# Performance work log

Measured on AMD Instinct MI355X. Metric: run time of the kernel, lower is better.

Reference implementation:

```python
import jax, jax.numpy as jnp
import numpy as np

DIM = 25
N_NODES = 20000
N_EDGES = 320000
NFEAT = 300
NHID = 64
NCLASS = 50


def setup_inputs() -> dict:
    key = jax.random.key(0)
    ks = jax.random.split(key, 8)
    s1 = np.sqrt(6.0 / (NFEAT + NHID))
    s2 = np.sqrt(6.0 / (NHID * DIM + NCLASS))
    return {
        "x": jax.random.normal(ks[0], (N_NODES, NFEAT), dtype=jnp.float32),
        "adj_rows": jax.random.randint(ks[1], (DIM, N_EDGES), 0, N_NODES, dtype=jnp.int32),
        "adj_cols": jax.random.randint(ks[2], (DIM, N_EDGES), 0, N_NODES, dtype=jnp.int32),
        "adj_vals": jax.random.uniform(ks[3], (DIM, N_EDGES), dtype=jnp.float32),
        "W1": jax.random.uniform(ks[4], (DIM, NFEAT, NHID), dtype=jnp.float32, minval=-s1, maxval=s1),
        "b1": jnp.zeros((DIM, NHID), dtype=jnp.float32),
        "W2": jax.random.uniform(ks[5], (DIM, NHID * DIM, NCLASS), dtype=jnp.float32, minval=-s2, maxval=s2),
        "b2": jnp.zeros((DIM, NCLASS), dtype=jnp.float32),
    }


def _spmm(rows, cols, vals, sup, n):
    # sparse [n,n] @ dense [n,f] via gather + segment-sum scatter-add
    return jax.ops.segment_sum(vals[:, None] * sup[cols], rows, num_segments=n)


def reference(x, adj_rows, adj_cols, adj_vals, W1, b1, W2, b2):
    n = x.shape[0]
    spmm = jax.vmap(lambda r, c, v, s: _spmm(r, c, v, s, n))
    # layer 1: per-branch dense mm, spmm, bias, relu  -> [DIM, n, NHID]
    sup1 = jnp.einsum("nf,dfh->dnh", x, W1)
    h1 = jax.nn.relu(spmm(adj_rows, adj_cols, adj_vals, sup1) + b1[:, None, :])
    # permute + reshape: concat branch features per node -> [n, DIM*NHID]
    h1cat = jnp.transpose(h1, (1, 0, 2)).reshape(n, -1)
    # layer 2: per-branch dense mm, spmm, bias, relu -> [DIM, n, NCLASS]
    sup2 = jnp.einsum("nk,dkc->dnc", h1cat, W2)
    h2 = jax.nn.relu(spmm(adj_rows, adj_cols, adj_vals, sup2) + b2[:, None, :])
    # max-pool over branches (POOLING='max')
    return jnp.max(h2, axis=0)
```

## Files before the change

### kernel.cpp

```cpp
#include <hip/hip_runtime.h>
#include <hip/hip_bf16.h>
#include <cstdint>
#include <cstddef>

#define DIM 25
#define NN 20000
#define NE 320000
#define NF 300
#define NH 64
#define NC 50
#define K2 (DIM*NH)
#define KP1 320
#define B1T_ROWS 1664
#define B2T_ROWS 1280
#define NBK 79
#define EPB 4096
#define BPB ((NE + EPB - 1) / EPB)
#define FCAP 5632

typedef __attribute__((ext_vector_type(8))) short short8;
typedef __attribute__((ext_vector_type(4))) float floatx4;
typedef __hip_bfloat16 bf16;

static __device__ __forceinline__ unsigned bf16bits(float f) {
    bf16 b = __float2bfloat16(f);
    return (unsigned)*reinterpret_cast<unsigned short*>(&b);
}
static __device__ __forceinline__ float blo(unsigned w) { return __uint_as_float(w << 16); }
static __device__ __forceinline__ float bhi(unsigned w) { return __uint_as_float(w & 0xFFFF0000u); }

static __device__ __forceinline__ void gld16(const void* g, void* l) {
    __builtin_amdgcn_global_load_lds((const __attribute__((address_space(1))) unsigned*)g,
                                     (__attribute__((address_space(3))) unsigned*)l, 16, 0, 0);
}

__global__ void zero_kernel(int* __restrict__ p, int n) {
    int i = blockIdx.x * blockDim.x + threadIdx.x;
    if (i < n) p[i] = 0;
}

__global__ __launch_bounds__(256) void bucket_scatter_kernel(const int* __restrict__ rows,
                                                             const int* __restrict__ cols,
                                                             const float* __restrict__ vals,
                                                             int* __restrict__ gcur,
                                                             unsigned* __restrict__ interE,
                                                             unsigned char* __restrict__ interR) {
    const int d = blockIdx.y;
    const int e0 = blockIdx.x * EPB;
    __shared__ int lh[NBK];
    __shared__ int lo[NBK];
    __shared__ int lbase[NBK];
    __shared__ unsigned entE[EPB];
    __shared__ unsigned short entR[EPB];
    const int tid = threadIdx.x;
    for (int i = tid; i < NBK; i += 256) lh[i] = 0;
    __syncthreads();
    const int* rd = rows + (size_t)d * NE;
    const int* cd = cols + (size_t)d * NE;
    const float* vd = vals + (size_t)d * NE;
    const int e1 = min(e0 + EPB, NE);
    const int ne = e1 - e0;
    for (int i = e0 + tid; i < e1; i += 256)
        atomicAdd(&lh[rd[i] >> 8], 1);
    __syncthreads();
    if (tid == 0) {
        int run = 0;
        for (int b = 0; b < NBK; ++b) { lo[b] = run; run += lh[b]; }
    }
    __syncthreads();
    for (int i = tid; i < NBK; i += 256) {
        lbase[i] = lh[i] ? atomicAdd(&gcur[d * NBK + i], lh[i]) : 0;
        lh[i] = 0;
    }
    __syncthreads();
    for (int i = e0 + tid; i < e1; i += 256) {
        int r = rd[i];
        int b = r >> 8;
        int rank = atomicAdd(&lh[b], 1);
        int pos = lo[b] + rank;
        entE[pos] = (unsigned)cd[i] | (bf16bits(vd[i]) << 16);
        entR[pos] = (unsigned short)r;
    }
    __syncthreads();
    for (int p = tid; p < ne; p += 256) {
        int r = entR[p];
        int b = r >> 8;
        int gpos = lbase[b] + (p - lo[b]);
        if (gpos < FCAP) {
            size_t slot = ((size_t)d * NBK + b) * FCAP + gpos;
            interE[slot] = entE[p];
            interR[slot] = (unsigned char)r;
        }
    }
}

__global__ void bucket_scan_kernel(const int* __restrict__ gcur,
                                   int* __restrict__ offs_b,
                                   int* __restrict__ bcnt,
                                   int* __restrict__ offs) {
    const int d = blockIdx.x;
    if (threadIdx.x != 0) return;
    int run = 0;
    for (int b = 0; b < NBK; ++b) {
        int c = min(gcur[d * NBK + b], FCAP);
        offs_b[d * NBK + b] = run;
        bcnt[d * NBK + b] = c;
        run += c;
    }
    offs[d * (NN + 1) + NN] = run;
}

__global__ __launch_bounds__(256) void csr_finalize_kernel(const unsigned* __restrict__ interE,
                                                           const unsigned char* __restrict__ interR,
                                                           const int* __restrict__ offs_b,
                                                           const int* __restrict__ bcnt,
                                                           int* __restrict__ offs,
                                                           unsigned* __restrict__ sedge) {
    const int d = blockIdx.y;
    const int b = blockIdx.x;
    const int tid = threadIdx.x;
    const int s = offs_b[d * NBK + b];
    const int cnt = bcnt[d * NBK + b];
    const size_t base = ((size_t)d * NBK + b) * FCAP;
    __shared__ int sm[256];
    __shared__ int cur[256];
    __shared__ unsigned lse[FCAP];
    sm[tid] = 0;
    __syncthreads();
    for (int i = tid; i < cnt; i += 256)
        atomicAdd(&sm[interR[base + i]], 1);
    __syncthreads();
    int own = sm[tid];
    for (int off = 1; off < 256; off <<= 1) {
        int t = (tid >= off) ? sm[tid - off] : 0;
        __syncthreads();
        sm[tid] += t;
        __syncthreads();
    }
    int excl = sm[tid] - own;
    int row = (b << 8) + tid;
    if (row < NN) offs[d * (NN + 1) + row] = s + excl;
    cur[tid] = excl;
    __syncthreads();
    for (int i = tid; i < cnt; i += 256) {
        int idx = atomicAdd(&cur[interR[base + i]], 1);
        lse[idx] = interE[base + i];
    }
    __syncthreads();
    unsigned* sed = sedge + (size_t)d * NE;
    for (int t = tid; t < cnt; t += 256)
        sed[s + t] = lse[t];
}

__global__ void pack_x_kernel(const float* __restrict__ x, bf16* __restrict__ xb) {
    int i = blockIdx.x * blockDim.x + threadIdx.x;
    if (i >= NN * KP1) return;
    int n = i / KP1, k = i - n * KP1;
    xb[i] = __float2bfloat16((k < NF) ? x[(size_t)n * NF + k] : 0.f);
}

__global__ void pack_b1_kernel(const float* __restrict__ W1, bf16* __restrict__ b1t) {
    int i = blockIdx.x * blockDim.x + threadIdx.x;
    if (i >= B1T_ROWS * KP1) return;
    int j2 = i / KP1, k = i - j2 * KP1;
    int chunk = j2 >> 9;
    int r = j2 & 511;
    int d = chunk * 8 + (r >> 6);
    float v = 0.f;
    if (d < DIM && k < NF)
        v = W1[(size_t)d * NF * NH + (size_t)k * NH + (r & 63)];
    b1t[i] = __float2bfloat16(v);
}

__global__ void pack_b2_kernel(const float* __restrict__ W2, bf16* __restrict__ b2t) {
    int i = blockIdx.x * blockDim.x + threadIdx.x;
    if (i >= B2T_ROWS * K2) return;
    int r = i / K2, k = i - r * K2;
    float v = 0.f;
    if (r < DIM * NC) {
        int g = r / NC, c = r - g * NC;
        v = W2[(size_t)g * K2 * NC + (size_t)k * NC + c];
    }
    b2t[i] = __float2bfloat16(v);
}

__global__ __launch_bounds__(256) void gemm_bf16_kernel(const bf16* __restrict__ A, int lda,
                                                        const bf16* __restrict__ BT, int ldb,
                                                        bf16* __restrict__ C,
                                                        int ksteps, int mode, int nvalid) {
    __shared__ unsigned short As[128 * 32];
    __shared__ unsigned short Bs[128 * 32];
    const int tid = threadIdx.x;
    const int wave = tid >> 6;
    const int lane = tid & 63;
    const int m0 = blockIdx.x * 128;
    const int n0 = blockIdx.y * 128;
    const int wm = (wave >> 1) * 64;
    const int wn = (wave & 1) * 64;
    floatx4 acc[4][4] = {};
    const int r0 = tid >> 2;
    const int kp = (tid & 3) * 8;
    const int q8 = (lane >> 4) * 8;
    unsigned short* lA0 = As + wave * 512;
    unsigned short* lA1 = As + 2048 + wave * 512;
    unsigned short* lB0 = Bs + wave * 512;
    unsigned short* lB1 = Bs + 2048 + wave * 512;
    const bf16* gA0 = A + (size_t)(m0 + r0) * lda + kp;
    const bf16* gA1 = A + (size_t)(m0 + r0 + 64) * lda + kp;
    const bf16* gB0 = BT + (size_t)(n0 + r0) * ldb + kp;
    const bf16* gB1 = BT + (size_t)(n0 + r0 + 64) * ldb + kp;

    for (int ks = 0; ks < ksteps; ++ks) {
        __syncthreads();
        gld16(gA0, lA0); gld16(gA1, lA1); gld16(gB0, lB0); gld16(gB1, lB1);
        gA0 += 32; gA1 += 32; gB0 += 32; gB1 += 32;
        __syncthreads();
        short8 af[4], bfr[4];
        #pragma unroll
        for (int i = 0; i < 4; ++i) {
            af[i]  = *(const short8*)&As[(wm + i * 16 + (lane & 15)) * 32 + q8];
            bfr[i] = *(const short8*)&Bs[(wn + i * 16 + (lane & 15)) * 32 + q8];
        }
        #pragma unroll
        for (int i = 0; i < 4; ++i)
            #pragma unroll
            for (int j = 0; j < 4; ++j)
                acc[i][j] = __builtin_amdgcn_mfma_f32_16x16x32_bf16(af[i], bfr[j], acc[i][j], 0, 0, 0);
    }
    const int cr = (lane >> 4) * 4;
    const int cc = lane & 15;
    #pragma unroll
    for (int i = 0; i < 4; ++i) {
        #pragma unroll
        for (int r = 0; r < 4; ++r) {
            int m = m0 + wm + i * 16 + cr + r;
            if (m >= NN) continue;
            #pragma unroll
            for (int j = 0; j < 4; ++j) {
                int n = n0 + wn + j * 16 + cc;
                if (n >= nvalid) continue;
                if (mode == 1) {
                    int g = n >> 6, h = n & 63;
                    C[(size_t)g * NN * NH + (size_t)m * NH + h] = __float2bfloat16(acc[i][j][r]);
                } else {
                    int g = n / NC, c = n - g * NC;
                    C[(size_t)g * NN * NC + (size_t)m * NC + c] = __float2bfloat16(acc[i][j][r]);
                }
            }
        }
    }
}

__global__ __launch_bounds__(256) void spmm1_kernel(const bf16* __restrict__ sup,
                                                    const int* __restrict__ offs,
                                                    const unsigned* __restrict__ sedge,
                                                    const float* __restrict__ b1,
                                                    bf16* __restrict__ h1cat, int d0, int CHk) {
    const int i = blockIdx.x;
    const int g = i % CHk;
    const int nb = i / CHk;
    const int tid = threadIdx.x;
    const int lane = tid & 63;
    const int n = nb * 8 + ((tid >> 6) << 1) + (lane >> 5);
    const int hl = lane & 31;
    const int d = d0 + g;
    const int s = offs[d * (NN + 1) + n];
    const int e = offs[d * (NN + 1) + n + 1];
    const char* supd = (const char*)sup + (size_t)g * NN * NH * 2;
    const unsigned* sed = sedge + (size_t)d * NE;
    const unsigned hoff = (unsigned)hl * 4;
    float alo0 = 0.f, ahi0 = 0.f, alo1 = 0.f, ahi1 = 0.f;
    int j = s;
    for (; j + 4 <= e; j += 4) {
        unsigned e0 = sed[j], e1 = sed[j + 1], e2 = sed[j + 2], e3 = sed[j + 3];
        unsigned w0 = *(const unsigned*)(supd + (((e0 & 0xFFFFu) << 7) | hoff));
        unsigned w1 = *(const unsigned*)(supd + (((e1 & 0xFFFFu) << 7) | hoff));
        unsigned w2 = *(const unsigned*)(supd + (((e2 & 0xFFFFu) << 7) | hoff));
        unsigned w3 = *(const unsigned*)(supd + (((e3 & 0xFFFFu) << 7) | hoff));
        float v0 = bhi(e0), v1 = bhi(e1), v2 = bhi(e2), v3 = bhi(e3);
        alo0 = fmaf(v0, blo(w0), alo0); ahi0 = fmaf(v0, bhi(w0), ahi0);
        alo1 = fmaf(v1, blo(w1), alo1); ahi1 = fmaf(v1, bhi(w1), ahi1);
        alo0 = fmaf(v2, blo(w2), alo0); ahi0 = fmaf(v2, bhi(w2), ahi0);
        alo1 = fmaf(v3, blo(w3), alo1); ahi1 = fmaf(v3, bhi(w3), ahi1);
    }
    for (; j < e; ++j) {
        unsigned e0 = sed[j];
        unsigned w0 = *(const unsigned*)(supd + (((e0 & 0xFFFFu) << 7) | hoff));
        float v0 = bhi(e0);
        alo0 = fmaf(v0, blo(w0), alo0); ahi0 = fmaf(v0, bhi(w0), ahi0);
    }
    float alo = fmaxf((alo0 + alo1) + b1[d * NH + 2 * hl], 0.f);
    float ahi = fmaxf((ahi0 + ahi1) + b1[d * NH + 2 * hl + 1], 0.f);
    unsigned packed = bf16bits(alo) | (bf16bits(ahi) << 16);
    *(unsigned*)((char*)h1cat + ((size_t)n * K2 + d * NH) * 2 + hoff) = packed;
}

__global__ __launch_bounds__(256) void spmm2b_kernel(const bf16* __restrict__ sup2,
                                                     const int* __restrict__ offs,
                                                     const unsigned* __restrict__ sedge,
                                                     const float* __restrict__ b2,
                                                     unsigned* __restrict__ h2u) {
    const int i = blockIdx.x;
    const int r = i & 7;
    const int q = i >> 3;
    int d, nb;
    if (q < 7500) { d = r + 8 * (q / 2500); nb = q % 2500; }
    else { d = 24; nb = (q - 7500) * 8 + r; if (nb >= 2500) return; }
    const int tid = threadIdx.x;
    const int lane = tid & 63;
    const int n = nb * 8 + ((tid >> 6) << 1) + (lane >> 5);
    const int cl = min(lane & 31, 24);
    const unsigned coff = (unsigned)cl * 4;
    const int s = offs[d * (NN + 1) + n];
    const int e = offs[d * (NN + 1) + n + 1];
    const char* supd = (const char*)sup2 + (size_t)d * NN * NC * 2;
    const unsigned* sed = sedge + (size_t)d * NE;
    float alo0 = b2[d * NC + 2 * cl], ahi0 = b2[d * NC + 2 * cl + 1];
    float alo1 = 0.f, ahi1 = 0.f;
    int j = s;
    for (; j + 4 <= e; j += 4) {
        unsigned e0 = sed[j], e1 = sed[j + 1], e2 = sed[j + 2], e3 = sed[j + 3];
        unsigned w0 = *(const unsigned*)(supd + ((e0 & 0xFFFFu) * 100u + coff));
        unsigned w1 = *(const unsigned*)(supd + ((e1 & 0xFFFFu) * 100u + coff));
        unsigned w2 = *(const unsigned*)(supd + ((e2 & 0xFFFFu) * 100u + coff));
        unsigned w3 = *(const unsigned*)(supd + ((e3 & 0xFFFFu) * 100u + coff));
        float v0 = bhi(e0), v1 = bhi(e1), v2 = bhi(e2), v3 = bhi(e3);
        alo0 = fmaf(v0, blo(w0), alo0); ahi0 = fmaf(v0, bhi(w0), ahi0);
        alo1 = fmaf(v1, blo(w1), alo1); ahi1 = fmaf(v1, bhi(w1), ahi1);
        alo0 = fmaf(v2, blo(w2), alo0); ahi0 = fmaf(v2, bhi(w2), ahi0);
        alo1 = fmaf(v3, blo(w3), alo1); ahi1 = fmaf(v3, bhi(w3), ahi1);
    }
    for (; j < e; ++j) {
        unsigned e0 = sed[j];
        unsigned w0 = *(const unsigned*)(supd + ((e0 & 0xFFFFu) * 100u + coff));
        float v0 = bhi(e0);
        alo0 = fmaf(v0, blo(w0), alo0); ahi0 = fmaf(v0, bhi(w0), ahi0);
    }
    float alo = fmaxf(alo0 + alo1, 0.f);
    float ahi = fmaxf(ahi0 + ahi1, 0.f);
    if ((lane & 31) < 25)
        h2u[((size_t)d * NN + n) * 25 + cl] = bf16bits(alo) | (bf16bits(ahi) << 16);
}

__global__ __launch_bounds__(256) void maxk_kernel(const unsigned* __restrict__ h2u,
                                                   float* __restrict__ out) {
    int i = blockIdx.x * blockDim.x + threadIdx.x;
    if (i >= NN * 25) return;
    int n = i / 25, cl = i - n * 25;
    float mlo = 0.f, mhi = 0.f;
    #pragma unroll
    for (int d = 0; d < DIM; ++d) {
        unsigned w = h2u[(size_t)d * NN * 25 + i];
        mlo = fmaxf(mlo, blo(w));
        mhi = fmaxf(mhi, bhi(w));
    }
    *(float2*)&out[(size_t)n * NC + 2 * cl] = make_float2(mlo, mhi);
}

extern "C" void kernel_launch(void* const* d_in, const int* in_sizes, int n_in,
                              void* d_out, int out_size, void* d_ws, size_t ws_size,
                              hipStream_t stream) {
    const float* x    = (const float*)d_in[0];
    const int*   rows = (const int*)d_in[1];
    const int*   cols = (const int*)d_in[2];
    const float* vals = (const float*)d_in[3];
    const float* W1   = (const float*)d_in[4];
    const float* b1   = (const float*)d_in[5];
    const float* W2   = (const float*)d_in[6];
    const float* b2   = (const float*)d_in[7];
    float* out = (float*)d_out;

    char* ws = (char*)d_ws;
    size_t off = 0;
    auto alloc = [&](size_t bytes) {
        void* p = ws + off;
        off += (bytes + 255) & ~(size_t)255;
        return p;
    };
    bf16* supbuf = (bf16*)alloc(sizeof(bf16) * (size_t)DIM * NN * NC);
    bf16* h1cat  = (bf16*)alloc(sizeof(bf16) * (size_t)NN * K2);
    bf16* b1t    = (bf16*)alloc(sizeof(bf16) * (size_t)B1T_ROWS * KP1);
    bf16* b2t    = (bf16*)alloc(sizeof(bf16) * (size_t)B2T_ROWS * K2);
    int*  offs   = (int*)alloc(sizeof(int) * (size_t)DIM * (NN + 1));
    int*  gcur   = (int*)alloc(sizeof(int) * (size_t)DIM * NBK);
    int*  offs_b = (int*)alloc(sizeof(int) * (size_t)DIM * NBK);
    int*  bcnt   = (int*)alloc(sizeof(int) * (size_t)DIM * NBK);
    unsigned* sedge = (unsigned*)alloc(sizeof(unsigned) * (size_t)DIM * NE);

    bf16* sup1 = supbuf;
    bf16* xbf  = supbuf + (size_t)12 * 1024 * 1024;
    bf16* sup2 = supbuf;
    unsigned* interE = (unsigned*)h1cat;
    unsigned char* interR = (unsigned char*)h1cat + (size_t)DIM * NBK * FCAP * 4;
    unsigned* h2u = (unsigned*)h1cat;

    if (off > ws_size) return;

    zero_kernel<<<(DIM * NBK + 255) / 256, 256, 0, stream>>>(gcur, DIM * NBK);
    bucket_scatter_kernel<<<dim3(BPB, DIM), 256, 0, stream>>>(rows, cols, vals, gcur, interE, interR);
    bucket_scan_kernel<<<DIM, 64, 0, stream>>>(gcur, offs_b, bcnt, offs);
    csr_finalize_kernel<<<dim3(NBK, DIM), 256, 0, stream>>>(interE, interR, offs_b, bcnt, offs, sedge);

    pack_x_kernel<<<(NN * KP1 + 255) / 256, 256, 0, stream>>>(x, xbf);
    pack_b1_kernel<<<(B1T_ROWS * KP1 + 255) / 256, 256, 0, stream>>>(W1, b1t);
    pack_b2_kernel<<<(B2T_ROWS * K2 + 255) / 256, 256, 0, stream>>>(W2, b2t);

    const int mtiles = (NN + 127) / 128;

    const int cstart[4] = {0, 8, 16, 24};
    const int csize[4]  = {8, 8, 8, 1};
    const int crow[4]   = {0, 512, 1024, 1536};
    for (int c = 0; c < 4; ++c) {
        int nv = csize[c] * 64;
        gemm_bf16_kernel<<<dim3(mtiles, (nv + 127) / 128), 256, 0, stream>>>(
            xbf, KP1, b1t + (size_t)crow[c] * KP1, KP1, sup1, KP1 / 32, 1, nv);
        spmm1_kernel<<<csize[c] * (NN / 8), 256, 0, stream>>>(
            sup1, offs, sedge, b1, h1cat, cstart[c], csize[c]);
    }
    gemm_bf16_kernel<<<dim3(mtiles, B2T_ROWS / 128), 256, 0, stream>>>(
        h1cat, K2, b2t, K2, sup2, K2 / 32, 2, DIM * NC);
    spmm2b_kernel<<<8 * 7813, 256, 0, stream>>>(sup2, offs, sedge, b2, h2u);
    maxk_kernel<<<(NN * 25 + 255) / 256, 256, 0, stream>>>(h2u, out);
}
```

Measured before the change: 778.8 us.

## Double-buffer GEMM LDS tiles, swizzle LDS layout, and group block rasterization

The bf16 GEMM kernel now uses two LDS buffers so the global-to-LDS load of the next K step is issued before the MFMA work on the current step, and one barrier per iteration replaces two. The LDS column groups are XOR-swizzled by row to reduce bank conflicts on the fragment reads. Blocks are also remapped into groups of eight M tiles for better L2 reuse of B. LDS use doubles, which may lower occupancy, and whether the overlap holds depends on how gld16 is synchronised.

```diff
diff --git a/kernel.cpp b/kernel.cpp
--- a/kernel.cpp
+++ b/kernel.cpp
@@ -188,44 +188,76 @@
                                                         const bf16* __restrict__ BT, int ldb,
                                                         bf16* __restrict__ C,
                                                         int ksteps, int mode, int nvalid) {
-    __shared__ unsigned short As[128 * 32];
-    __shared__ unsigned short Bs[128 * 32];
+    __shared__ unsigned short As[2 * 128 * 32];
+    __shared__ unsigned short Bs[2 * 128 * 32];
     const int tid = threadIdx.x;
     const int wave = tid >> 6;
     const int lane = tid & 63;
-    const int m0 = blockIdx.x * 128;
-    const int n0 = blockIdx.y * 128;
+
+    const int mtiles = (int)gridDim.x;
+    const int ntiles = (int)gridDim.y;
+    const int bid = (int)blockIdx.y * mtiles + (int)blockIdx.x;
+    const int per_group = 8 * ntiles;
+    const int group = bid / per_group;
+    const int rem = bid - group * per_group;
+    const int first_m = group * 8;
+    const int gm = min(8, mtiles - first_m);
+    const int mt = first_m + rem % gm;
+    const int nt = rem / gm;
+    const int m0 = mt * 128;
+    const int n0 = nt * 128;
+
     const int wm = (wave >> 1) * 64;
     const int wn = (wave & 1) * 64;
     floatx4 acc[4][4] = {};
     const int r0 = tid >> 2;
-    const int kp = (tid & 3) * 8;
+    const int cg = (tid & 3) ^ ((r0 >> 1) & 3);
     const int q8 = (lane >> 4) * 8;
+    const int gq = q8 >> 3;
     unsigned short* lA0 = As + wave * 512;
     unsigned short* lA1 = As + 2048 + wave * 512;
     unsigned short* lB0 = Bs + wave * 512;
     unsigned short* lB1 = Bs + 2048 + wave * 512;
-    const bf16* gA0 = A + (size_t)(m0 + r0) * lda + kp;
-    const bf16* gA1 = A + (size_t)(m0 + r0 + 64) * lda + kp;
-    const bf16* gB0 = BT + (size_t)(n0 + r0) * ldb + kp;
-    const bf16* gB1 = BT + (size_t)(n0 + r0 + 64) * ldb + kp;
-
+    const bf16* gA0 = A + (size_t)(m0 + r0) * lda + cg * 8;
+    const bf16* gA1 = A + (size_t)(m0 + r0 + 64) * lda + cg * 8;
+    const bf16* gB0 = BT + (size_t)(n0 + r0) * ldb + cg * 8;
+    const bf16* gB1 = BT + (size_t)(n0 + r0 + 64) * ldb + cg * 8;
+
+    int offA[4], offB[4];
+    #pragma unroll
+    for (int i = 0; i < 4; ++i) {
+        int ra = wm + i * 16 + (lane & 15);
+        int rb = wn + i * 16 + (lane & 15);
+        offA[i] = ra * 32 + ((gq ^ ((ra >> 1) & 3)) << 3);
+        offB[i] = rb * 32 + ((gq ^ ((rb >> 1) & 3)) << 3);
+    }
+
+    gld16(gA0, lA0); gld16(gA1, lA1); gld16(gB0, lB0); gld16(gB1, lB1);
+    __syncthreads();
+
+    int cur = 0;
     for (int ks = 0; ks < ksteps; ++ks) {
-        __syncthreads();
-        gld16(gA0, lA0); gld16(gA1, lA1); gld16(gB0, lB0); gld16(gB1, lB1);
-        gA0 += 32; gA1 += 32; gB0 += 32; gB1 += 32;
-        __syncthreads();
+        if (ks + 1 < ksteps) {
+            const int nb = cur ^ 1;
+            const size_t ko = (size_t)(ks + 1) * 32;
+            gld16(gA0 + ko, lA0 + nb * 4096); gld16(gA1 + ko, lA1 + nb * 4096);
+            gld16(gB0 + ko, lB0 + nb * 4096); gld16(gB1 + ko, lB1 + nb * 4096);
+        }
+        const unsigned short* as = As + cur * 4096;
+        const unsigned short* bs = Bs + cur * 4096;
         short8 af[4], bfr[4];
         #pragma unroll
         for (int i = 0; i < 4; ++i) {
-            af[i]  = *(const short8*)&As[(wm + i * 16 + (lane & 15)) * 32 + q8];
-            bfr[i] = *(const short8*)&Bs[(wn + i * 16 + (lane & 15)) * 32 + q8];
+            af[i]  = *(const short8*)&as[offA[i]];
+            bfr[i] = *(const short8*)&bs[offB[i]];
         }
         #pragma unroll
         for (int i = 0; i < 4; ++i)
             #pragma unroll
             for (int j = 0; j < 4; ++j)
                 acc[i][j] = __builtin_amdgcn_mfma_f32_16x16x32_bf16(af[i], bfr[j], acc[i][j], 0, 0, 0);
+        __syncthreads();
+        cur ^= 1;
     }
     const int cr = (lane >> 4) * 4;
     const int cc = lane & 15;
```

Result: faster. 757.2 us (-2.8%).
